# Optimization experiments

Hardware: AMD Instinct MI355X
Metric: run time of the kernel (lower is better)

Reference implementation:

```python
import jax, jax.numpy as jnp
import numpy as np

H = 256          # hidden_dim
ITERS = 3        # num_routing_iterations
# directed level pairs (src != tgt), torch iteration order over 3 levels:
SRC = jnp.array([0, 0, 1, 1, 2, 2])
TGT = jnp.array([1, 2, 0, 2, 0, 1])


def _ln(x, g, b, eps=1e-5):
    mu = x.mean(-1, keepdims=True)
    var = ((x - mu) ** 2).mean(-1, keepdims=True)
    return (x - mu) / jnp.sqrt(var + eps) * g + b


def setup_inputs() -> dict:
    key = jax.random.key(0)
    ks = iter(jax.random.split(key, 24))
    B = 32768
    lin = lambda k, fin, fout: jax.random.normal(k, (fin, fout), jnp.float32) / np.sqrt(fin).astype(np.float32)
    return {
        'x_fine':   jax.random.normal(next(ks), (B, 128), jnp.float32),
        'x_medium': jax.random.normal(next(ks), (B, 256), jnp.float32),
        'x_coarse': jax.random.normal(next(ks), (B, 512), jnp.float32),
        # per-level input projections (dims differ, so separate)
        'pW0': lin(next(ks), 128, H), 'pb0': jnp.zeros((H,), jnp.float32),
        'pW1': lin(next(ks), 256, H), 'pb1': jnp.zeros((H,), jnp.float32),
        'pW2': lin(next(ks), 512, H), 'pb2': jnp.zeros((H,), jnp.float32),
        # routing MLPs, stacked over the 6 directed pairs
        'rW1': jax.random.normal(next(ks), (6, 2 * H, H), jnp.float32) / np.sqrt(2 * H).astype(np.float32),
        'rb1': jnp.zeros((6, H), jnp.float32),
        'rW2': jax.random.normal(next(ks), (6, H, 1), jnp.float32) / np.sqrt(H).astype(np.float32),
        'rb2': jnp.zeros((6, 1), jnp.float32),
        # per-level processors, stacked over 3 levels
        'lpW1': jax.random.normal(next(ks), (3, H, H), jnp.float32) / np.sqrt(H).astype(np.float32),
        'lpb1': jnp.zeros((3, H), jnp.float32),
        'lpW2': jax.random.normal(next(ks), (3, H, H), jnp.float32) / np.sqrt(H).astype(np.float32),
        'lpb2': jnp.zeros((3, H), jnp.float32),
        'lng': jnp.ones((3, H), jnp.float32), 'lnb': jnp.zeros((3, H), jnp.float32),
        # final aggregator
        'faW1': jax.random.normal(next(ks), (3 * H, H), jnp.float32) / np.sqrt(3 * H).astype(np.float32),
        'fab1': jnp.zeros((H,), jnp.float32),
        'faW2': jax.random.normal(next(ks), (H, H), jnp.float32) / np.sqrt(H).astype(np.float32),
        'fab2': jnp.zeros((H,), jnp.float32),
        'fng': jnp.ones((H,), jnp.float32), 'fnb': jnp.zeros((H,), jnp.float32),
    }


def _forward(x_fine, x_medium, x_coarse, pW0, pb0, pW1, pb1, pW2, pb2,
             rW1, rb1, rW2, rb2, lpW1, lpb1, lpW2, lpb2, lng, lnb,
             faW1, fab1, faW2, fab2, fng, fnb):
    # project each level to hidden dim -> [3, B, H]
    feats = jnp.stack([x_fine @ pW0 + pb0,
                       x_medium @ pW1 + pb1,
                       x_coarse @ pW2 + pb2])
    w = None
    for _ in range(ITERS):  # fixed small routing-iteration loop
        src = feats[SRC]                                      # [6, B, H]
        tgt = feats[TGT]                                      # [6, B, H]
        comb = jnp.concatenate([src, tgt], axis=-1)           # [6, B, 2H]
        h = jax.nn.relu(jnp.einsum('pbd,pdh->pbh', comb, rW1) + rb1[:, None, :])
        w = jax.nn.sigmoid(jnp.einsum('pbh,pho->pbo', h, rW2) + rb2[:, None, :])  # [6, B, 1]
        # scatter routed features into target levels (weighted sum)
        agg = jax.ops.segment_sum(w * src, TGT, num_segments=3)  # [3, B, H]
        upd = feats + agg
        # per-level processor MLP + LayerNorm (dropout in eval mode = identity)
        h2 = jax.nn.relu(jnp.einsum('lbd,lde->lbe', upd, lpW1) + lpb1[:, None, :])
        h3 = jnp.einsum('lbd,lde->lbe', h2, lpW2) + lpb2[:, None, :]
        feats = _ln(h3, lng[:, None, :], lnb[:, None, :])
    B = feats.shape[1]
    cat = jnp.transpose(feats, (1, 0, 2)).reshape(B, 3 * H)  # level order matches torch cat
    h4 = jax.nn.relu(cat @ faW1 + fab1)
    out = _ln(h4 @ faW2 + fab2, fng, fnb)
    return out, w


def reference(x_fine, x_medium, x_coarse, pW0, pb0, pW1, pb1, pW2, pb2,
              rW1, rb1, rW2, rb2, lpW1, lpb1, lpW2, lpb2, lng, lnb,
              faW1, fab1, faW2, fab2, fng, fnb):
    return _forward(x_fine, x_medium, x_coarse, pW0, pb0, pW1, pb1, pW2, pb2,
                    rW1, rb1, rW2, rb2, lpW1, lpb1, lpW2, lpb2, lng, lnb,
                    faW1, fab1, faW2, fab2, fng, fnb)
```

## Files before the change

kernel.cpp:

```cpp
#include <hip/hip_runtime.h>
#include <math.h>

typedef __bf16 bf16;
typedef __bf16 bf16x8 __attribute__((ext_vector_type(8)));
typedef __bf16 bf16x4 __attribute__((ext_vector_type(4)));
typedef float f32x4 __attribute__((ext_vector_type(4)));

#define B_ROWS 32768
#define PSZ 8192
#define PBYTES 16384

#define PB_PW0   0
#define PB_PW1   4
#define PB_PW2   12
#define PB_RW1   28
#define PB_LPW1  124
#define PB_LPW2  148
#define PB_FAW1  172
#define PB_FAW2  196

__global__ void wprep_kernel(const float* __restrict__ pW0, const float* __restrict__ pW1,
                             const float* __restrict__ pW2, const float* __restrict__ rW1,
                             const float* __restrict__ lpW1, const float* __restrict__ lpW2,
                             const float* __restrict__ faW1, const float* __restrict__ faW2,
                             bf16* __restrict__ ws) {
  int p = blockIdx.x;
  const float* src; int kp;
  if (p < 4)        { src = pW0;  kp = p; }
  else if (p < 12)  { src = pW1;  kp = p - 4; }
  else if (p < 28)  { src = pW2;  kp = p - 12; }
  else if (p < 124) { int q = p - 28;  src = rW1  + (size_t)(q >> 4) * 512 * 256; kp = q & 15; }
  else if (p < 148) { int q = p - 124; src = lpW1 + (size_t)(q >> 3) * 256 * 256; kp = q & 7; }
  else if (p < 172) { int q = p - 148; src = lpW2 + (size_t)(q >> 3) * 256 * 256; kp = q & 7; }
  else if (p < 196) { src = faW1; kp = p - 172; }
  else              { src = faW2; kp = p - 196; }
  bf16* dst = ws + (size_t)p * PSZ;
  int n = threadIdx.x;
#pragma unroll
  for (int kb = 0; kb < 32; kb += 8) {
    bf16x8 v;
#pragma unroll
    for (int j = 0; j < 8; j++)
      v[j] = (bf16)src[(size_t)(kp * 32 + kb + j) * 256 + n];
    *(bf16x8*)(dst + n * 32 + kb) = v;
  }
}

#define FENCE asm volatile("" ::: "memory")
#define BAR()  do { FENCE; __builtin_amdgcn_s_barrier(); FENCE; } while (0)
#define BARP() do { asm volatile("s_waitcnt lgkmcnt(0)" ::: "memory"); \
                    __builtin_amdgcn_s_barrier(); FENCE; } while (0)
#define VWB2(N, B) asm volatile("s_waitcnt vmcnt(" #N ")" \
                                : "+v"(B[0]), "+v"(B[1]) :: "memory")
#define VWB4(N, B) asm volatile("s_waitcnt vmcnt(" #N ")" \
                                : "+v"(B[0]), "+v"(B[1]), "+v"(B[2]), "+v"(B[3]) :: "memory")

__device__ __forceinline__ void ld2(bf16x8& d0, bf16x8& d1, const void* addr) {
  asm volatile("global_load_dwordx4 %0, %2, off\n\t"
               "global_load_dwordx4 %1, %2, off offset:1024"
               : "=&v"(d0), "=&v"(d1)
               : "v"(addr));
}
__device__ __forceinline__ void ld4(bf16x8& d0, bf16x8& d1, bf16x8& d2, bf16x8& d3,
                                    const void* addr) {
  asm volatile("global_load_dwordx4 %0, %4, off\n\t"
               "global_load_dwordx4 %1, %4, off offset:1024\n\t"
               "global_load_dwordx4 %2, %4, off offset:2048\n\t"
               "global_load_dwordx4 %3, %4, off offset:3072"
               : "=&v"(d0), "=&v"(d1), "=&v"(d2), "=&v"(d3)
               : "v"(addr));
}

__global__ void __launch_bounds__(512)
__attribute__((amdgpu_waves_per_eu(2, 2)))
fused_kernel(const float* __restrict__ xf, const float* __restrict__ xm,
                  const float* __restrict__ xc,
                  const float* __restrict__ pb0, const float* __restrict__ pb1v,
                  const float* __restrict__ pb2v,
                  const float* __restrict__ rb1, const float* __restrict__ rW2,
                  const float* __restrict__ rb2,
                  const float* __restrict__ lpb1, const float* __restrict__ lpb2,
                  const float* __restrict__ lng, const float* __restrict__ lnb,
                  const float* __restrict__ fab1, const float* __restrict__ fab2,
                  const float* __restrict__ fng, const float* __restrict__ fnb,
                  const bf16* __restrict__ ws, float* __restrict__ out) {
  __shared__ bf16 feats[3][64][256];
  __shared__ bf16 apan[64][32];
  __shared__ float w_route[6][64];
  __shared__ float lnred[8][2][64];

  const int t = threadIdx.x;
  const int lane = t & 63;
  const int cg = t >> 6;
  const int lr = lane & 15;
  const int lk = lane >> 4;
  const int r0 = blockIdx.x * 64;

  char* featsB = (char*)&feats[0][0][0];
  char* apanB  = (char*)&apan[0][0];

  f32x4 acc[16];
  auto zacc16 = [&]() {
#pragma unroll
    for (int i = 0; i < 16; i++) acc[i] = (f32x4){0.f, 0.f, 0.f, 0.f};
  };
  auto zacc8 = [&]() {
#pragma unroll
    for (int i = 0; i < 8; i++) acc[i] = (f32x4){0.f, 0.f, 0.f, 0.f};
  };

  auto mf = [&](bf16x8* Av, bf16x8* Bv) {
    __builtin_amdgcn_s_setprio(1);
#pragma unroll
    for (int rt = 0; rt < 4; rt++)
#pragma unroll
      for (int ct = 0; ct < 2; ct++)
        acc[rt * 2 + ct] = __builtin_amdgcn_mfma_f32_16x16x32_bf16(Av[rt], Bv[ct], acc[rt * 2 + ct], 0, 0, 0);
    __builtin_amdgcn_s_setprio(0);
  };
  auto mfR = [&](bf16x8* Av, bf16x8* Bv) {
    __builtin_amdgcn_s_setprio(1);
#pragma unroll
    for (int rt = 0; rt < 4; rt++)
#pragma unroll
      for (int ct = 0; ct < 4; ct++)
        acc[rt * 4 + ct] = __builtin_amdgcn_mfma_f32_16x16x32_bf16(Av[rt], Bv[ct], acc[rt * 4 + ct], 0, 0, 0);
    __builtin_amdgcn_s_setprio(0);
  };

  const int SRCa[6] = {0, 0, 1, 1, 2, 2};
  const int TGTa[6] = {1, 2, 0, 2, 0, 1};

  auto gemmR = [&](int p0) {
    const int pp = p0 + (cg >> 2);
    const char* Wb = (const char*)(ws + (size_t)(PB_RW1 + pp * 16) * PSZ)
                     + (((cg & 3) * 64 + lr) * 64 + lk * 16);
    const int lS = SRCa[p0];
    const int lT = TGTa[pp];
    bf16x8 Ba[4], Bb[4], Aa[4], Ab[4];
    auto ldB = [&](int s, bf16x8* Bv) {
      ld4(Bv[0], Bv[1], Bv[2], Bv[3], Wb + (size_t)s * PBYTES);
    };
    auto readA = [&](int s, bf16x8* Av) {
      int lvl = (s < 8) ? lS : lT;
      int q = (s & 7) * 4;
#pragma unroll
      for (int rt = 0; rt < 4; rt++) {
        int r = rt * 16 + lr;
        Av[rt] = *(const bf16x8*)(featsB + ((lvl * 64 + r) << 9) + (((q + lk) ^ (r & 7)) << 4));
      }
    };
    ldB(0, Ba); ldB(1, Bb);
    readA(0, Aa);
    int s = 0;
#pragma unroll 1
    for (; s < 14; s += 2) {
      readA(s + 1, Ab); VWB4(4, Ba); mfR(Aa, Ba); ldB(s + 2, Ba);
      readA(s + 2, Aa); VWB4(4, Bb); mfR(Ab, Bb); ldB(s + 3, Bb);
    }
    readA(15, Ab); VWB4(4, Ba); mfR(Aa, Ba);
    VWB4(0, Bb); mfR(Ab, Bb);
  };

  auto routing_epi2 = [&](int p0) {
    const int pp = p0 + (cg >> 2);
    float part[4][4] = {{0}};
#pragma unroll
    for (int ct = 0; ct < 4; ct++) {
      int col = (cg & 3) * 64 + ct * 16 + lr;
      float b1 = rb1[pp * 256 + col];
      float w2 = rW2[pp * 256 + col];
#pragma unroll
      for (int rt = 0; rt < 4; rt++)
#pragma unroll
        for (int e = 0; e < 4; e++)
          part[rt][e] += fmaxf(acc[rt * 4 + ct][e] + b1, 0.f) * w2;
    }
#pragma unroll
    for (int m = 1; m < 16; m <<= 1)
#pragma unroll
      for (int rt = 0; rt < 4; rt++)
#pragma unroll
        for (int e = 0; e < 4; e++)
          part[rt][e] += __shfl_xor(part[rt][e], m, 64);
    if (lr == 0)
#pragma unroll
      for (int rt = 0; rt < 4; rt++)
#pragma unroll
        for (int e = 0; e < 4; e++)
          lnred[cg][0][rt * 16 + lk * 4 + e] = part[rt][e];
    BARP();
    if (t < 128) {
      int pi = t >> 6, r = t & 63;
      float s = rb2[p0 + pi];
#pragma unroll
      for (int g = 0; g < 4; g++) s += lnred[pi * 4 + g][0][r];
      w_route[p0 + pi][r] = 1.f / (1.f + expf(-s));
    }
    BARP();
  };

  auto gemm = [&](const bf16* W, int n, int l0, int l1, int l2) {
    const char* Wb = (const char*)W + ((cg * 32 + lr) * 64 + lk * 16);
    bf16x8 B0[2], B1[2], B2[2], B3[2], A0[4], A1[4];
    auto ldB = [&](int s, bf16x8* Bv) {
      ld2(Bv[0], Bv[1], Wb + (size_t)s * PBYTES);
    };
    auto readA = [&](int s, bf16x8* Av) {
      int lvl = (s >= 16) ? l2 : ((s >= 8) ? l1 : l0);
      int q = (s & 7) * 4;
#pragma unroll
      for (int rt = 0; rt < 4; rt++) {
        int r = rt * 16 + lr;
        Av[rt] = *(const bf16x8*)(featsB + ((lvl * 64 + r) << 9) + (((q + lk) ^ (r & 7)) << 4));
      }
    };
    ldB(0, B0); ldB(1, B1); ldB(2, B2); ldB(3, B3);
    readA(0, A0);
    int s = 0;
#pragma unroll 1
    for (; s < n - 4; s += 4) {
      readA(s + 1, A1); VWB2(6, B0); mf(A0, B0); ldB(s + 4, B0);
      readA(s + 2, A0); VWB2(6, B1); mf(A1, B1); ldB(s + 5, B1);
      readA(s + 3, A1); VWB2(6, B2); mf(A0, B2); ldB(s + 6, B2);
      readA(s + 4, A0); VWB2(6, B3); mf(A1, B3); ldB(s + 7, B3);
    }
    readA(s + 1, A1); VWB2(6, B0); mf(A0, B0);
    readA(s + 2, A0); VWB2(4, B1); mf(A1, B1);
    readA(s + 3, A1); VWB2(2, B2); mf(A0, B2);
    VWB2(0, B3); mf(A1, B3);
  };

  auto gemm_x = [&](const bf16* W, int n, const float* X, int Kx) {
    const char* Wb = (const char*)W + ((cg * 32 + lr) * 64 + lk * 16);
#pragma unroll 1
    for (int s = 0; s < n; s++) {
      bf16x8 b[2];
#pragma unroll
      for (int ct = 0; ct < 2; ct++)
        b[ct] = *(const bf16x8*)(Wb + (size_t)s * PBYTES + ct * 1024);
      int rr = t >> 3, c0 = (t & 7) * 4;
      float4 xv = *(const float4*)(X + (size_t)(r0 + rr) * Kx + s * 32 + c0);
      BAR();
      bf16x4 v;
      v[0] = (bf16)xv.x; v[1] = (bf16)xv.y; v[2] = (bf16)xv.z; v[3] = (bf16)xv.w;
      int cb = c0 >> 3;
      *(bf16x4*)(apanB + (rr << 6) + ((cb ^ ((rr >> 1) & 3)) << 4) + (c0 & 7) * 2) = v;
      BARP();
      bf16x8 a[4];
#pragma unroll
      for (int rt = 0; rt < 4; rt++) {
        int r = rt * 16 + lr;
        a[rt] = *(const bf16x8*)(apanB + (r << 6) + ((lk ^ ((r >> 1) & 3)) << 4));
      }
      mf(a, b);
    }
  };

  auto stF = [&](int lvl, int r, int c, float v) {
    *(bf16*)(featsB + ((lvl * 64 + r) << 9) +
             ((((c >> 3) ^ (r & 7))) << 4) + (c & 7) * 2) = (bf16)v;
  };
  auto epi_bias_store = [&](const float* bias, int lvl, bool do_relu) {
    BAR();
#pragma unroll
    for (int ct = 0; ct < 2; ct++) {
      int col = cg * 32 + ct * 16 + lr;
      float bv = bias[col];
#pragma unroll
      for (int rt = 0; rt < 4; rt++)
#pragma unroll
        for (int e = 0; e < 4; e++) {
          float v = acc[rt * 2 + ct][e] + bv;
          if (do_relu) v = fmaxf(v, 0.f);
          stF(lvl, rt * 16 + lk * 4 + e, col, v);
        }
    }
    BARP();
  };
  auto ln_epi = [&](const float* bias, const float* gamma, const float* beta, int lvl) {
    float sum[4][4] = {{0}}, sq[4][4] = {{0}};
#pragma unroll
    for (int ct = 0; ct < 2; ct++) {
      int col = cg * 32 + ct * 16 + lr;
      float bv = bias[col];
#pragma unroll
      for (int rt = 0; rt < 4; rt++)
#pragma unroll
        for (int e = 0; e < 4; e++) {
          float v = acc[rt * 2 + ct][e] + bv;
          acc[rt * 2 + ct][e] = v;
          sum[rt][e] += v; sq[rt][e] += v * v;
        }
    }
#pragma unroll
    for (int m = 1; m < 16; m <<= 1)
#pragma unroll
      for (int rt = 0; rt < 4; rt++)
#pragma unroll
        for (int e = 0; e < 4; e++) {
          sum[rt][e] += __shfl_xor(sum[rt][e], m, 64);
          sq[rt][e]  += __shfl_xor(sq[rt][e], m, 64);
        }
    if (lr == 0)
#pragma unroll
      for (int rt = 0; rt < 4; rt++)
#pragma unroll
        for (int e = 0; e < 4; e++) {
          int r = rt * 16 + lk * 4 + e;
          lnred[cg][0][r] = sum[rt][e];
          lnred[cg][1][r] = sq[rt][e];
        }
    BARP();
    if (t < 64) {
      float su = 0.f, sz = 0.f;
#pragma unroll
      for (int g = 0; g < 8; g++) { su += lnred[g][0][t]; sz += lnred[g][1][t]; }
      float mu = su * (1.f / 256.f);
      float ms = sz * (1.f / 256.f);
      lnred[0][0][t] = mu;
      lnred[0][1][t] = rsqrtf(ms - mu * mu + 1e-5f);
    }
    BARP();
#pragma unroll
    for (int rt = 0; rt < 4; rt++)
#pragma unroll
      for (int e = 0; e < 4; e++) {
        int r = rt * 16 + lk * 4 + e;
        float mu = lnred[0][0][r];
        float rstd = lnred[0][1][r];
#pragma unroll
        for (int ct = 0; ct < 2; ct++) {
          int col = cg * 32 + ct * 16 + lr;
          float v = (acc[rt * 2 + ct][e] - mu) * rstd * gamma[col] + beta[col];
          if (lvl >= 0) stF(lvl, r, col, v);
          else out[(size_t)(r0 + r) * 256 + col] = v;
        }
      }
    BARP();
  };

  zacc8(); gemm_x(ws + PB_PW0 * PSZ, 4,  xf, 128); epi_bias_store(pb0, 0, false);
  zacc8(); gemm_x(ws + PB_PW1 * PSZ, 8,  xm, 256); epi_bias_store(pb1v, 1, false);
  zacc8(); gemm_x(ws + PB_PW2 * PSZ, 16, xc, 512); epi_bias_store(pb2v, 2, false);

  for (int it = 0; it < 3; it++) {
    for (int p0 = 0; p0 < 6; p0 += 2) {
      zacc16();
      gemmR(p0);
      routing_epi2(p0);
    }
    {
      int r = t >> 3, c0 = (t & 7) * 32;
      float w6[6];
#pragma unroll
      for (int p = 0; p < 6; p++) w6[p] = w_route[p][r];
#pragma unroll
      for (int ccx = 0; ccx < 32; ccx += 8) {
        int c = c0 + ccx;
        int chunk = (((c >> 3) ^ (r & 7)) << 4);
        char* a0 = featsB + ((0 * 64 + r) << 9) + chunk;
        char* a1 = featsB + ((1 * 64 + r) << 9) + chunk;
        char* a2 = featsB + ((2 * 64 + r) << 9) + chunk;
        bf16x8 f0 = *(bf16x8*)a0, f1 = *(bf16x8*)a1, f2 = *(bf16x8*)a2;
        bf16x8 u0, u1, u2;
#pragma unroll
        for (int i = 0; i < 8; i++) {
          float a = (float)f0[i], b = (float)f1[i], d = (float)f2[i];
          u0[i] = (bf16)(a + w6[2] * b + w6[4] * d);
          u1[i] = (bf16)(b + w6[0] * a + w6[5] * d);
          u2[i] = (bf16)(d + w6[1] * a + w6[3] * b);
        }
        *(bf16x8*)a0 = u0; *(bf16x8*)a1 = u1; *(bf16x8*)a2 = u2;
      }
      BARP();
    }
    for (int l = 0; l < 3; l++) {
      zacc8();
      gemm(ws + (PB_LPW1 + l * 8) * PSZ, 8, l, 0, 0);
      epi_bias_store(lpb1 + l * 256, l, true);
      zacc8();
      gemm(ws + (PB_LPW2 + l * 8) * PSZ, 8, l, 0, 0);
      ln_epi(lpb2 + l * 256, lng + l * 256, lnb + l * 256, l);
    }
  }

  zacc8();
  gemm(ws + PB_FAW1 * PSZ, 24, 0, 1, 2);
  epi_bias_store(fab1, 0, true);
  zacc8();
  gemm(ws + PB_FAW2 * PSZ, 8, 0, 0, 0);
  ln_epi(fab2, fng, fnb, -1);

  if (t < 384) {
    int p = t >> 6, r = t & 63;
    out[(size_t)B_ROWS * 256 + (size_t)p * B_ROWS + r0 + r] = w_route[p][r];
  }
}

extern "C" void kernel_launch(void* const* d_in, const int* in_sizes, int n_in,
                              void* d_out, int out_size, void* d_ws, size_t ws_size,
                              hipStream_t stream) {
  const float* xf   = (const float*)d_in[0];
  const float* xm   = (const float*)d_in[1];
  const float* xc   = (const float*)d_in[2];
  const float* pW0  = (const float*)d_in[3];
  const float* pb0  = (const float*)d_in[4];
  const float* pW1  = (const float*)d_in[5];
  const float* pb1  = (const float*)d_in[6];
  const float* pW2  = (const float*)d_in[7];
  const float* pb2  = (const float*)d_in[8];
  const float* rW1  = (const float*)d_in[9];
  const float* rb1  = (const float*)d_in[10];
  const float* rW2  = (const float*)d_in[11];
  const float* rb2  = (const float*)d_in[12];
  const float* lpW1 = (const float*)d_in[13];
  const float* lpb1 = (const float*)d_in[14];
  const float* lpW2 = (const float*)d_in[15];
  const float* lpb2 = (const float*)d_in[16];
  const float* lng  = (const float*)d_in[17];
  const float* lnb  = (const float*)d_in[18];
  const float* faW1 = (const float*)d_in[19];
  const float* fab1 = (const float*)d_in[20];
  const float* faW2 = (const float*)d_in[21];
  const float* fab2 = (const float*)d_in[22];
  const float* fng  = (const float*)d_in[23];
  const float* fnb  = (const float*)d_in[24];
  (void)in_sizes; (void)n_in; (void)out_size; (void)ws_size;

  bf16* ws = (bf16*)d_ws;
  float* out = (float*)d_out;

  wprep_kernel<<<204, 256, 0, stream>>>(pW0, pW1, pW2, rW1, lpW1, lpW2, faW1, faW2, ws);
  fused_kernel<<<512, 512, 0, stream>>>(xf, xm, xc, pb0, pb1, pb2, rb1, rW2, rb2,
                                        lpb1, lpb2, lng, lnb, fab1, fab2, fng, fnb,
                                        ws, out);
}
```

Baseline: 425.9 us.

## Halve row tile to 32 rows per block to double occupancy

```diff
diff --git a/kernel.cpp b/kernel.cpp
--- a/kernel.cpp
+++ b/kernel.cpp
@@ -4,6 +4,7 @@
 typedef __bf16 bf16;
 typedef __bf16 bf16x8 __attribute__((ext_vector_type(8)));
 typedef __bf16 bf16x4 __attribute__((ext_vector_type(4)));
+typedef __bf16 bf16x2 __attribute__((ext_vector_type(2)));
 typedef float f32x4 __attribute__((ext_vector_type(4)));
 
 #define B_ROWS 32768
@@ -72,7 +73,7 @@
 }
 
 __global__ void __launch_bounds__(512)
-__attribute__((amdgpu_waves_per_eu(2, 2)))
+__attribute__((amdgpu_waves_per_eu(4, 4)))
 fused_kernel(const float* __restrict__ xf, const float* __restrict__ xm,
                   const float* __restrict__ xc,
                   const float* __restrict__ pb0, const float* __restrict__ pb1v,
@@ -84,35 +85,35 @@
                   const float* __restrict__ fab1, const float* __restrict__ fab2,
                   const float* __restrict__ fng, const float* __restrict__ fnb,
                   const bf16* __restrict__ ws, float* __restrict__ out) {
-  __shared__ bf16 feats[3][64][256];
-  __shared__ bf16 apan[64][32];
-  __shared__ float w_route[6][64];
-  __shared__ float lnred[8][2][64];
+  __shared__ bf16 feats[3][32][256];
+  __shared__ char scratch[2048];
+  __shared__ float w_route[6][32];
 
   const int t = threadIdx.x;
   const int lane = t & 63;
   const int cg = t >> 6;
   const int lr = lane & 15;
   const int lk = lane >> 4;
-  const int r0 = blockIdx.x * 64;
+  const int r0 = blockIdx.x * 32;
 
   char* featsB = (char*)&feats[0][0][0];
-  char* apanB  = (char*)&apan[0][0];
-
-  f32x4 acc[16];
-  auto zacc16 = [&]() {
-#pragma unroll
-    for (int i = 0; i < 16; i++) acc[i] = (f32x4){0.f, 0.f, 0.f, 0.f};
-  };
+  char* apanB  = scratch;
+  float (*lnred)[2][32] = (float (*)[2][32])scratch;
+
+  f32x4 acc[8];
   auto zacc8 = [&]() {
 #pragma unroll
     for (int i = 0; i < 8; i++) acc[i] = (f32x4){0.f, 0.f, 0.f, 0.f};
+  };
+  auto zacc4 = [&]() {
+#pragma unroll
+    for (int i = 0; i < 4; i++) acc[i] = (f32x4){0.f, 0.f, 0.f, 0.f};
   };
 
   auto mf = [&](bf16x8* Av, bf16x8* Bv) {
     __builtin_amdgcn_s_setprio(1);
 #pragma unroll
-    for (int rt = 0; rt < 4; rt++)
+    for (int rt = 0; rt < 2; rt++)
 #pragma unroll
       for (int ct = 0; ct < 2; ct++)
         acc[rt * 2 + ct] = __builtin_amdgcn_mfma_f32_16x16x32_bf16(Av[rt], Bv[ct], acc[rt * 2 + ct], 0, 0, 0);
@@ -121,7 +122,7 @@
   auto mfR = [&](bf16x8* Av, bf16x8* Bv) {
     __builtin_amdgcn_s_setprio(1);
 #pragma unroll
-    for (int rt = 0; rt < 4; rt++)
+    for (int rt = 0; rt < 2; rt++)
 #pragma unroll
       for (int ct = 0; ct < 4; ct++)
         acc[rt * 4 + ct] = __builtin_amdgcn_mfma_f32_16x16x32_bf16(Av[rt], Bv[ct], acc[rt * 4 + ct], 0, 0, 0);
@@ -137,7 +138,7 @@
                      + (((cg & 3) * 64 + lr) * 64 + lk * 16);
     const int lS = SRCa[p0];
     const int lT = TGTa[pp];
-    bf16x8 Ba[4], Bb[4], Aa[4], Ab[4];
+    bf16x8 Ba[4], Bb[4], Aa[2], Ab[2];
     auto ldB = [&](int s, bf16x8* Bv) {
       ld4(Bv[0], Bv[1], Bv[2], Bv[3], Wb + (size_t)s * PBYTES);
     };
@@ -145,9 +146,9 @@
       int lvl = (s < 8) ? lS : lT;
       int q = (s & 7) * 4;
 #pragma unroll
-      for (int rt = 0; rt < 4; rt++) {
+      for (int rt = 0; rt < 2; rt++) {
         int r = rt * 16 + lr;
-        Av[rt] = *(const bf16x8*)(featsB + ((lvl * 64 + r) << 9) + (((q + lk) ^ (r & 7)) << 4));
+        Av[rt] = *(const bf16x8*)(featsB + ((lvl * 32 + r) << 9) + (((q + lk) ^ (r & 7)) << 4));
       }
     };
     ldB(0, Ba); ldB(1, Bb);
@@ -164,14 +165,14 @@
 
   auto routing_epi2 = [&](int p0) {
     const int pp = p0 + (cg >> 2);
-    float part[4][4] = {{0}};
+    float part[2][4] = {{0}};
 #pragma unroll
     for (int ct = 0; ct < 4; ct++) {
       int col = (cg & 3) * 64 + ct * 16 + lr;
       float b1 = rb1[pp * 256 + col];
       float w2 = rW2[pp * 256 + col];
 #pragma unroll
-      for (int rt = 0; rt < 4; rt++)
+      for (int rt = 0; rt < 2; rt++)
 #pragma unroll
         for (int e = 0; e < 4; e++)
           part[rt][e] += fmaxf(acc[rt * 4 + ct][e] + b1, 0.f) * w2;
@@ -179,19 +180,19 @@
 #pragma unroll
     for (int m = 1; m < 16; m <<= 1)
 #pragma unroll
-      for (int rt = 0; rt < 4; rt++)
+      for (int rt = 0; rt < 2; rt++)
 #pragma unroll
         for (int e = 0; e < 4; e++)
           part[rt][e] += __shfl_xor(part[rt][e], m, 64);
     if (lr == 0)
 #pragma unroll
-      for (int rt = 0; rt < 4; rt++)
+      for (int rt = 0; rt < 2; rt++)
 #pragma unroll
         for (int e = 0; e < 4; e++)
           lnred[cg][0][rt * 16 + lk * 4 + e] = part[rt][e];
     BARP();
-    if (t < 128) {
-      int pi = t >> 6, r = t & 63;
+    if (t < 64) {
+      int pi = t >> 5, r = t & 31;
       float s = rb2[p0 + pi];
 #pragma unroll
       for (int g = 0; g < 4; g++) s += lnred[pi * 4 + g][0][r];
@@ -202,7 +203,7 @@
 
   auto gemm = [&](const bf16* W, int n, int l0, int l1, int l2) {
     const char* Wb = (const char*)W + ((cg * 32 + lr) * 64 + lk * 16);
-    bf16x8 B0[2], B1[2], B2[2], B3[2], A0[4], A1[4];
+    bf16x8 B0[2], B1[2], B2[2], B3[2], A0[2], A1[2];
     auto ldB = [&](int s, bf16x8* Bv) {
       ld2(Bv[0], Bv[1], Wb + (size_t)s * PBYTES);
     };
@@ -210,9 +211,9 @@
       int lvl = (s >= 16) ? l2 : ((s >= 8) ? l1 : l0);
       int q = (s & 7) * 4;
 #pragma unroll
-      for (int rt = 0; rt < 4; rt++) {
+      for (int rt = 0; rt < 2; rt++) {
         int r = rt * 16 + lr;
-        Av[rt] = *(const bf16x8*)(featsB + ((lvl * 64 + r) << 9) + (((q + lk) ^ (r & 7)) << 4));
+        Av[rt] = *(const bf16x8*)(featsB + ((lvl * 32 + r) << 9) + (((q + lk) ^ (r & 7)) << 4));
       }
     };
     ldB(0, B0); ldB(1, B1); ldB(2, B2); ldB(3, B3);
@@ -239,17 +240,17 @@
 #pragma unroll
       for (int ct = 0; ct < 2; ct++)
         b[ct] = *(const bf16x8*)(Wb + (size_t)s * PBYTES + ct * 1024);
-      int rr = t >> 3, c0 = (t & 7) * 4;
-      float4 xv = *(const float4*)(X + (size_t)(r0 + rr) * Kx + s * 32 + c0);
+      int rr = t >> 4, c0 = (t & 15) * 2;
+      float2 xv = *(const float2*)(X + (size_t)(r0 + rr) * Kx + s * 32 + c0);
       BAR();
-      bf16x4 v;
-      v[0] = (bf16)xv.x; v[1] = (bf16)xv.y; v[2] = (bf16)xv.z; v[3] = (bf16)xv.w;
+      bf16x2 v;
+      v[0] = (bf16)xv.x; v[1] = (bf16)xv.y;
       int cb = c0 >> 3;
-      *(bf16x4*)(apanB + (rr << 6) + ((cb ^ ((rr >> 1) & 3)) << 4) + (c0 & 7) * 2) = v;
+      *(bf16x2*)(apanB + (rr << 6) + ((cb ^ ((rr >> 1) & 3)) << 4) + (c0 & 7) * 2) = v;
       BARP();
-      bf16x8 a[4];
-#pragma unroll
-      for (int rt = 0; rt < 4; rt++) {
+      bf16x8 a[2];
+#pragma unroll
+      for (int rt = 0; rt < 2; rt++) {
         int r = rt * 16 + lr;
         a[rt] = *(const bf16x8*)(apanB + (r << 6) + ((lk ^ ((r >> 1) & 3)) << 4));
       }
@@ -258,7 +259,7 @@
   };
 
   auto stF = [&](int lvl, int r, int c, float v) {
-    *(bf16*)(featsB + ((lvl * 64 + r) << 9) +
+    *(bf16*)(featsB + ((lvl * 32 + r) << 9) +
              ((((c >> 3) ^ (r & 7))) << 4) + (c & 7) * 2) = (bf16)v;
   };
   auto epi_bias_store = [&](const float* bias, int lvl, bool do_relu) {
@@ -268,7 +269,7 @@
       int col = cg * 32 + ct * 16 + lr;
       float bv = bias[col];
 #pragma unroll
-      for (int rt = 0; rt < 4; rt++)
+      for (int rt = 0; rt < 2; rt++)
 #pragma unroll
         for (int e = 0; e < 4; e++) {
           float v = acc[rt * 2 + ct][e] + bv;
@@ -279,13 +280,13 @@
     BARP();
   };
   auto ln_epi = [&](const float* bias, const float* gamma, const float* beta, int lvl) {
-    float sum[4][4] = {{0}}, sq[4][4] = {{0}};
+    float sum[2][4] = {{0}}, sq[2][4] = {{0}};
 #pragma unroll
     for (int ct = 0; ct < 2; ct++) {
       int col = cg * 32 + ct * 16 + lr;
       float bv = bias[col];
 #pragma unroll
-      for (int rt = 0; rt < 4; rt++)
+      for (int rt = 0; rt < 2; rt++)
 #pragma unroll
         for (int e = 0; e < 4; e++) {
           float v = acc[rt * 2 + ct][e] + bv;
@@ -296,15 +297,15 @@
 #pragma unroll
     for (int m = 1; m < 16; m <<= 1)
 #pragma unroll
-      for (int rt = 0; rt < 4; rt++)
-#pragma unroll
-        for (int e = 0; e < 4; e++) {
+      for (int rt = 0; rt < 2; rt++)
+#pragma unroll
+      for (int e = 0; e < 4; e++) {
           sum[rt][e] += __shfl_xor(sum[rt][e], m, 64);
           sq[rt][e]  += __shfl_xor(sq[rt][e], m, 64);
         }
     if (lr == 0)
 #pragma unroll
-      for (int rt = 0; rt < 4; rt++)
+      for (int rt = 0; rt < 2; rt++)
 #pragma unroll
         for (int e = 0; e < 4; e++) {
           int r = rt * 16 + lk * 4 + e;
@@ -312,7 +313,7 @@
           lnred[cg][1][r] = sq[rt][e];
         }
     BARP();
-    if (t < 64) {
+    if (t < 32) {
       float su = 0.f, sz = 0.f;
 #pragma unroll
       for (int g = 0; g < 8; g++) { su += lnred[g][0][t]; sz += lnred[g][1][t]; }
@@ -323,7 +324,7 @@
     }
     BARP();
 #pragma unroll
-    for (int rt = 0; rt < 4; rt++)
+    for (int rt = 0; rt < 2; rt++)
 #pragma unroll
       for (int e = 0; e < 4; e++) {
         int r = rt * 16 + lk * 4 + e;
@@ -340,28 +341,28 @@
     BARP();
   };
 
-  zacc8(); gemm_x(ws + PB_PW0 * PSZ, 4,  xf, 128); epi_bias_store(pb0, 0, false);
-  zacc8(); gemm_x(ws + PB_PW1 * PSZ, 8,  xm, 256); epi_bias_store(pb1v, 1, false);
-  zacc8(); gemm_x(ws + PB_PW2 * PSZ, 16, xc, 512); epi_bias_store(pb2v, 2, false);
+  zacc4(); gemm_x(ws + PB_PW0 * PSZ, 4,  xf, 128); epi_bias_store(pb0, 0, false);
+  zacc4(); gemm_x(ws + PB_PW1 * PSZ, 8,  xm, 256); epi_bias_store(pb1v, 1, false);
+  zacc4(); gemm_x(ws + PB_PW2 * PSZ, 16, xc, 512); epi_bias_store(pb2v, 2, false);
 
   for (int it = 0; it < 3; it++) {
     for (int p0 = 0; p0 < 6; p0 += 2) {
-      zacc16();
+      zacc8();
       gemmR(p0);
       routing_epi2(p0);
     }
     {
-      int r = t >> 3, c0 = (t & 7) * 32;
+      int r = t >> 4, c0 = (t & 15) * 16;
       float w6[6];
 #pragma unroll
       for (int p = 0; p < 6; p++) w6[p] = w_route[p][r];
 #pragma unroll
-      for (int ccx = 0; ccx < 32; ccx += 8) {
+      for (int ccx = 0; ccx < 16; ccx += 8) {
         int c = c0 + ccx;
         int chunk = (((c >> 3) ^ (r & 7)) << 4);
-        char* a0 = featsB + ((0 * 64 + r) << 9) + chunk;
-        char* a1 = featsB + ((1 * 64 + r) << 9) + chunk;
-        char* a2 = featsB + ((2 * 64 + r) << 9) + chunk;
+        char* a0 = featsB + ((0 * 32 + r) << 9) + chunk;
+        char* a1 = featsB + ((1 * 32 + r) << 9) + chunk;
+        char* a2 = featsB + ((2 * 32 + r) << 9) + chunk;
         bf16x8 f0 = *(bf16x8*)a0, f1 = *(bf16x8*)a1, f2 = *(bf16x8*)a2;
         bf16x8 u0, u1, u2;
 #pragma unroll
@@ -376,24 +377,24 @@
       BARP();
     }
     for (int l = 0; l < 3; l++) {
-      zacc8();
+      zacc4();
       gemm(ws + (PB_LPW1 + l * 8) * PSZ, 8, l, 0, 0);
       epi_bias_store(lpb1 + l * 256, l, true);
-      zacc8();
+      zacc4();
       gemm(ws + (PB_LPW2 + l * 8) * PSZ, 8, l, 0, 0);
       ln_epi(lpb2 + l * 256, lng + l * 256, lnb + l * 256, l);
     }
   }
 
-  zacc8();
+  zacc4();
   gemm(ws + PB_FAW1 * PSZ, 24, 0, 1, 2);
   epi_bias_store(fab1, 0, true);
-  zacc8();
+  zacc4();
   gemm(ws + PB_FAW2 * PSZ, 8, 0, 0, 0);
   ln_epi(fab2, fng, fnb, -1);
 
-  if (t < 384) {
-    int p = t >> 6, r = t & 63;
+  if (t < 192) {
+    int p = t >> 5, r = t & 31;
     out[(size_t)B_ROWS * 256 + (size_t)p * B_ROWS + r0 + r] = w_route[p][r];
   }
 }
@@ -432,7 +433,7 @@
   float* out = (float*)d_out;
 
   wprep_kernel<<<204, 256, 0, stream>>>(pW0, pW1, pW2, rW1, lpW1, lpW2, faW1, faW2, ws);
-  fused_kernel<<<512, 512, 0, stream>>>(xf, xm, xc, pb0, pb1, pb2, rb1, rW2, rb2,
-                                        lpb1, lpb2, lng, lnb, fab1, fab2, fng, fnb,
-                                        ws, out);
+  fused_kernel<<<1024, 512, 0, stream>>>(xf, xm, xc, pb0, pb1, pb2, rb1, rW2, rb2,
+                                         lpb1, lpb2, lng, lnb, fab1, fab2, fng, fnb,
+                                         ws, out);
 }
```

Result: slower. 636.2 us (+49.4%).

## Shrink per-block row tile to 48 and relax waves-per-EU bound

Applied to the files above, without the earlier changes.

```diff
diff --git a/kernel.cpp b/kernel.cpp
--- a/kernel.cpp
+++ b/kernel.cpp
@@ -7,6 +7,7 @@
 typedef float f32x4 __attribute__((ext_vector_type(4)));
 
 #define B_ROWS 32768
+#define ROWS 48
 #define PSZ 8192
 #define PBYTES 16384
 
@@ -72,7 +73,7 @@
 }
 
 __global__ void __launch_bounds__(512)
-__attribute__((amdgpu_waves_per_eu(2, 2)))
+__attribute__((amdgpu_waves_per_eu(2, 4)))
 fused_kernel(const float* __restrict__ xf, const float* __restrict__ xm,
                   const float* __restrict__ xc,
                   const float* __restrict__ pb0, const float* __restrict__ pb1v,
@@ -84,35 +85,35 @@
                   const float* __restrict__ fab1, const float* __restrict__ fab2,
                   const float* __restrict__ fng, const float* __restrict__ fnb,
                   const bf16* __restrict__ ws, float* __restrict__ out) {
-  __shared__ bf16 feats[3][64][256];
-  __shared__ bf16 apan[64][32];
-  __shared__ float w_route[6][64];
-  __shared__ float lnred[8][2][64];
+  __shared__ bf16 feats[3][ROWS][256];
+  __shared__ char scratch[3072];
+  __shared__ float w_route[6][ROWS];
 
   const int t = threadIdx.x;
   const int lane = t & 63;
   const int cg = t >> 6;
   const int lr = lane & 15;
   const int lk = lane >> 4;
-  const int r0 = blockIdx.x * 64;
+  const int r0 = blockIdx.x * ROWS;
 
   char* featsB = (char*)&feats[0][0][0];
-  char* apanB  = (char*)&apan[0][0];
-
-  f32x4 acc[16];
-  auto zacc16 = [&]() {
-#pragma unroll
-    for (int i = 0; i < 16; i++) acc[i] = (f32x4){0.f, 0.f, 0.f, 0.f};
-  };
-  auto zacc8 = [&]() {
-#pragma unroll
-    for (int i = 0; i < 8; i++) acc[i] = (f32x4){0.f, 0.f, 0.f, 0.f};
+  char* apanB  = scratch;
+  float (*lnred)[2][ROWS] = (float (*)[2][ROWS])scratch;
+
+  f32x4 acc[12];
+  auto zacc12 = [&]() {
+#pragma unroll
+    for (int i = 0; i < 12; i++) acc[i] = (f32x4){0.f, 0.f, 0.f, 0.f};
+  };
+  auto zacc6 = [&]() {
+#pragma unroll
+    for (int i = 0; i < 6; i++) acc[i] = (f32x4){0.f, 0.f, 0.f, 0.f};
   };
 
   auto mf = [&](bf16x8* Av, bf16x8* Bv) {
     __builtin_amdgcn_s_setprio(1);
 #pragma unroll
-    for (int rt = 0; rt < 4; rt++)
+    for (int rt = 0; rt < 3; rt++)
 #pragma unroll
       for (int ct = 0; ct < 2; ct++)
         acc[rt * 2 + ct] = __builtin_amdgcn_mfma_f32_16x16x32_bf16(Av[rt], Bv[ct], acc[rt * 2 + ct], 0, 0, 0);
@@ -121,7 +122,7 @@
   auto mfR = [&](bf16x8* Av, bf16x8* Bv) {
     __builtin_amdgcn_s_setprio(1);
 #pragma unroll
-    for (int rt = 0; rt < 4; rt++)
+    for (int rt = 0; rt < 3; rt++)
 #pragma unroll
       for (int ct = 0; ct < 4; ct++)
         acc[rt * 4 + ct] = __builtin_amdgcn_mfma_f32_16x16x32_bf16(Av[rt], Bv[ct], acc[rt * 4 + ct], 0, 0, 0);
@@ -137,7 +138,7 @@
                      + (((cg & 3) * 64 + lr) * 64 + lk * 16);
     const int lS = SRCa[p0];
     const int lT = TGTa[pp];
-    bf16x8 Ba[4], Bb[4], Aa[4], Ab[4];
+    bf16x8 Ba[4], Bb[4], Aa[3], Ab[3];
     auto ldB = [&](int s, bf16x8* Bv) {
       ld4(Bv[0], Bv[1], Bv[2], Bv[3], Wb + (size_t)s * PBYTES);
     };
@@ -145,9 +146,9 @@
       int lvl = (s < 8) ? lS : lT;
       int q = (s & 7) * 4;
 #pragma unroll
-      for (int rt = 0; rt < 4; rt++) {
+      for (int rt = 0; rt < 3; rt++) {
         int r = rt * 16 + lr;
-        Av[rt] = *(const bf16x8*)(featsB + ((lvl * 64 + r) << 9) + (((q + lk) ^ (r & 7)) << 4));
+        Av[rt] = *(const bf16x8*)(featsB + ((lvl * ROWS + r) << 9) + (((q + lk) ^ (r & 7)) << 4));
       }
     };
     ldB(0, Ba); ldB(1, Bb);
@@ -164,14 +165,14 @@
 
   auto routing_epi2 = [&](int p0) {
     const int pp = p0 + (cg >> 2);
-    float part[4][4] = {{0}};
+    float part[3][4] = {{0}};
 #pragma unroll
     for (int ct = 0; ct < 4; ct++) {
       int col = (cg & 3) * 64 + ct * 16 + lr;
       float b1 = rb1[pp * 256 + col];
       float w2 = rW2[pp * 256 + col];
 #pragma unroll
-      for (int rt = 0; rt < 4; rt++)
+      for (int rt = 0; rt < 3; rt++)
 #pragma unroll
         for (int e = 0; e < 4; e++)
           part[rt][e] += fmaxf(acc[rt * 4 + ct][e] + b1, 0.f) * w2;
@@ -179,19 +180,19 @@
 #pragma unroll
     for (int m = 1; m < 16; m <<= 1)
 #pragma unroll
-      for (int rt = 0; rt < 4; rt++)
+      for (int rt = 0; rt < 3; rt++)
 #pragma unroll
         for (int e = 0; e < 4; e++)
           part[rt][e] += __shfl_xor(part[rt][e], m, 64);
     if (lr == 0)
 #pragma unroll
-      for (int rt = 0; rt < 4; rt++)
+      for (int rt = 0; rt < 3; rt++)
 #pragma unroll
         for (int e = 0; e < 4; e++)
           lnred[cg][0][rt * 16 + lk * 4 + e] = part[rt][e];
     BARP();
-    if (t < 128) {
-      int pi = t >> 6, r = t & 63;
+    if (t < 2 * ROWS) {
+      int pi = t / ROWS, r = t % ROWS;
       float s = rb2[p0 + pi];
 #pragma unroll
       for (int g = 0; g < 4; g++) s += lnred[pi * 4 + g][0][r];
@@ -202,7 +203,7 @@
 
   auto gemm = [&](const bf16* W, int n, int l0, int l1, int l2) {
     const char* Wb = (const char*)W + ((cg * 32 + lr) * 64 + lk * 16);
-    bf16x8 B0[2], B1[2], B2[2], B3[2], A0[4], A1[4];
+    bf16x8 B0[2], B1[2], B2[2], B3[2], A0[3], A1[3];
     auto ldB = [&](int s, bf16x8* Bv) {
       ld2(Bv[0], Bv[1], Wb + (size_t)s * PBYTES);
     };
@@ -210,9 +211,9 @@
       int lvl = (s >= 16) ? l2 : ((s >= 8) ? l1 : l0);
       int q = (s & 7) * 4;
 #pragma unroll
-      for (int rt = 0; rt < 4; rt++) {
+      for (int rt = 0; rt < 3; rt++) {
         int r = rt * 16 + lr;
-        Av[rt] = *(const bf16x8*)(featsB + ((lvl * 64 + r) << 9) + (((q + lk) ^ (r & 7)) << 4));
+        Av[rt] = *(const bf16x8*)(featsB + ((lvl * ROWS + r) << 9) + (((q + lk) ^ (r & 7)) << 4));
       }
     };
     ldB(0, B0); ldB(1, B1); ldB(2, B2); ldB(3, B3);
@@ -233,23 +234,26 @@
 
   auto gemm_x = [&](const bf16* W, int n, const float* X, int Kx) {
     const char* Wb = (const char*)W + ((cg * 32 + lr) * 64 + lk * 16);
+    int rr = t >> 3, c0 = (t & 7) * 4;
+    int row = r0 + rr; if (row > B_ROWS - 1) row = B_ROWS - 1;
 #pragma unroll 1
     for (int s = 0; s < n; s++) {
       bf16x8 b[2];
 #pragma unroll
       for (int ct = 0; ct < 2; ct++)
         b[ct] = *(const bf16x8*)(Wb + (size_t)s * PBYTES + ct * 1024);
-      int rr = t >> 3, c0 = (t & 7) * 4;
-      float4 xv = *(const float4*)(X + (size_t)(r0 + rr) * Kx + s * 32 + c0);
+      float4 xv = *(const float4*)(X + (size_t)row * Kx + s * 32 + c0);
       BAR();
-      bf16x4 v;
-      v[0] = (bf16)xv.x; v[1] = (bf16)xv.y; v[2] = (bf16)xv.z; v[3] = (bf16)xv.w;
-      int cb = c0 >> 3;
-      *(bf16x4*)(apanB + (rr << 6) + ((cb ^ ((rr >> 1) & 3)) << 4) + (c0 & 7) * 2) = v;
+      if (rr < ROWS) {
+        bf16x4 v;
+        v[0] = (bf16)xv.x; v[1] = (bf16)xv.y; v[2] = (bf16)xv.z; v[3] = (bf16)xv.w;
+        int cb = c0 >> 3;
+        *(bf16x4*)(apanB + (rr << 6) + ((cb ^ ((rr >> 1) & 3)) << 4) + (c0 & 7) * 2) = v;
+      }
       BARP();
-      bf16x8 a[4];
-#pragma unroll
-      for (int rt = 0; rt < 4; rt++) {
+      bf16x8 a[3];
+#pragma unroll
+      for (int rt = 0; rt < 3; rt++) {
         int r = rt * 16 + lr;
         a[rt] = *(const bf16x8*)(apanB + (r << 6) + ((lk ^ ((r >> 1) & 3)) << 4));
       }
@@ -258,7 +262,7 @@
   };
 
   auto stF = [&](int lvl, int r, int c, float v) {
-    *(bf16*)(featsB + ((lvl * 64 + r) << 9) +
+    *(bf16*)(featsB + ((lvl * ROWS + r) << 9) +
              ((((c >> 3) ^ (r & 7))) << 4) + (c & 7) * 2) = (bf16)v;
   };
   auto epi_bias_store = [&](const float* bias, int lvl, bool do_relu) {
@@ -268,7 +272,7 @@
       int col = cg * 32 + ct * 16 + lr;
       float bv = bias[col];
 #pragma unroll
-      for (int rt = 0; rt < 4; rt++)
+      for (int rt = 0; rt < 3; rt++)
 #pragma unroll
         for (int e = 0; e < 4; e++) {
           float v = acc[rt * 2 + ct][e] + bv;
@@ -279,13 +283,13 @@
     BARP();
   };
   auto ln_epi = [&](const float* bias, const float* gamma, const float* beta, int lvl) {
-    float sum[4][4] = {{0}}, sq[4][4] = {{0}};
+    float sum[3][4] = {{0}}, sq[3][4] = {{0}};
 #pragma unroll
     for (int ct = 0; ct < 2; ct++) {
       int col = cg * 32 + ct * 16 + lr;
       float bv = bias[col];
 #pragma unroll
-      for (int rt = 0; rt < 4; rt++)
+      for (int rt = 0; rt < 3; rt++)
 #pragma unroll
         for (int e = 0; e < 4; e++) {
           float v = acc[rt * 2 + ct][e] + bv;
@@ -296,7 +300,7 @@
 #pragma unroll
     for (int m = 1; m < 16; m <<= 1)
 #pragma unroll
-      for (int rt = 0; rt < 4; rt++)
+      for (int rt = 0; rt < 3; rt++)
 #pragma unroll
         for (int e = 0; e < 4; e++) {
           sum[rt][e] += __shfl_xor(sum[rt][e], m, 64);
@@ -304,7 +308,7 @@
         }
     if (lr == 0)
 #pragma unroll
-      for (int rt = 0; rt < 4; rt++)
+      for (int rt = 0; rt < 3; rt++)
 #pragma unroll
         for (int e = 0; e < 4; e++) {
           int r = rt * 16 + lk * 4 + e;
@@ -312,7 +316,7 @@
           lnred[cg][1][r] = sq[rt][e];
         }
     BARP();
-    if (t < 64) {
+    if (t < ROWS) {
       float su = 0.f, sz = 0.f;
 #pragma unroll
       for (int g = 0; g < 8; g++) { su += lnred[g][0][t]; sz += lnred[g][1][t]; }
@@ -323,7 +327,7 @@
     }
     BARP();
 #pragma unroll
-    for (int rt = 0; rt < 4; rt++)
+    for (int rt = 0; rt < 3; rt++)
 #pragma unroll
       for (int e = 0; e < 4; e++) {
         int r = rt * 16 + lk * 4 + e;
@@ -334,67 +338,70 @@
           int col = cg * 32 + ct * 16 + lr;
           float v = (acc[rt * 2 + ct][e] - mu) * rstd * gamma[col] + beta[col];
           if (lvl >= 0) stF(lvl, r, col, v);
-          else out[(size_t)(r0 + r) * 256 + col] = v;
-        }
-      }
-    BARP();
-  };
-
-  zacc8(); gemm_x(ws + PB_PW0 * PSZ, 4,  xf, 128); epi_bias_store(pb0, 0, false);
-  zacc8(); gemm_x(ws + PB_PW1 * PSZ, 8,  xm, 256); epi_bias_store(pb1v, 1, false);
-  zacc8(); gemm_x(ws + PB_PW2 * PSZ, 16, xc, 512); epi_bias_store(pb2v, 2, false);
+          else if (r0 + r < B_ROWS) out[(size_t)(r0 + r) * 256 + col] = v;
+        }
+      }
+    BARP();
+  };
+
+  zacc6(); gemm_x(ws + PB_PW0 * PSZ, 4,  xf, 128); epi_bias_store(pb0, 0, false);
+  zacc6(); gemm_x(ws + PB_PW1 * PSZ, 8,  xm, 256); epi_bias_store(pb1v, 1, false);
+  zacc6(); gemm_x(ws + PB_PW2 * PSZ, 16, xc, 512); epi_bias_store(pb2v, 2, false);
 
   for (int it = 0; it < 3; it++) {
     for (int p0 = 0; p0 < 6; p0 += 2) {
-      zacc16();
+      zacc12();
       gemmR(p0);
       routing_epi2(p0);
     }
     {
       int r = t >> 3, c0 = (t & 7) * 32;
-      float w6[6];
-#pragma unroll
-      for (int p = 0; p < 6; p++) w6[p] = w_route[p][r];
-#pragma unroll
-      for (int ccx = 0; ccx < 32; ccx += 8) {
-        int c = c0 + ccx;
-        int chunk = (((c >> 3) ^ (r & 7)) << 4);
-        char* a0 = featsB + ((0 * 64 + r) << 9) + chunk;
-        char* a1 = featsB + ((1 * 64 + r) << 9) + chunk;
-        char* a2 = featsB + ((2 * 64 + r) << 9) + chunk;
-        bf16x8 f0 = *(bf16x8*)a0, f1 = *(bf16x8*)a1, f2 = *(bf16x8*)a2;
-        bf16x8 u0, u1, u2;
-#pragma unroll
-        for (int i = 0; i < 8; i++) {
-          float a = (float)f0[i], b = (float)f1[i], d = (float)f2[i];
-          u0[i] = (bf16)(a + w6[2] * b + w6[4] * d);
-          u1[i] = (bf16)(b + w6[0] * a + w6[5] * d);
-          u2[i] = (bf16)(d + w6[1] * a + w6[3] * b);
-        }
-        *(bf16x8*)a0 = u0; *(bf16x8*)a1 = u1; *(bf16x8*)a2 = u2;
+      if (r < ROWS) {
+        float w6[6];
+#pragma unroll
+        for (int p = 0; p < 6; p++) w6[p] = w_route[p][r];
+#pragma unroll
+        for (int ccx = 0; ccx < 32; ccx += 8) {
+          int c = c0 + ccx;
+          int chunk = (((c >> 3) ^ (r & 7)) << 4);
+          char* a0 = featsB + ((0 * ROWS + r) << 9) + chunk;
+          char* a1 = featsB + ((1 * ROWS + r) << 9) + chunk;
+          char* a2 = featsB + ((2 * ROWS + r) << 9) + chunk;
+          bf16x8 f0 = *(bf16x8*)a0, f1 = *(bf16x8*)a1, f2 = *(bf16x8*)a2;
+          bf16x8 u0, u1, u2;
+#pragma unroll
+          for (int i = 0; i < 8; i++) {
+            float a = (float)f0[i], b = (float)f1[i], d = (float)f2[i];
+            u0[i] = (bf16)(a + w6[2] * b + w6[4] * d);
+            u1[i] = (bf16)(b + w6[0] * a + w6[5] * d);
+            u2[i] = (bf16)(d + w6[1] * a + w6[3] * b);
+          }
+          *(bf16x8*)a0 = u0; *(bf16x8*)a1 = u1; *(bf16x8*)a2 = u2;
+        }
       }
       BARP();
     }
     for (int l = 0; l < 3; l++) {
-      zacc8();
+      zacc6();
       gemm(ws + (PB_LPW1 + l * 8) * PSZ, 8, l, 0, 0);
       epi_bias_store(lpb1 + l * 256, l, true);
-      zacc8();
+      zacc6();
       gemm(ws + (PB_LPW2 + l * 8) * PSZ, 8, l, 0, 0);
       ln_epi(lpb2 + l * 256, lng + l * 256, lnb + l * 256, l);
     }
   }
 
-  zacc8();
+  zacc6();
   gemm(ws + PB_FAW1 * PSZ, 24, 0, 1, 2);
   epi_bias_store(fab1, 0, true);
-  zacc8();
+  zacc6();
   gemm(ws + PB_FAW2 * PSZ, 8, 0, 0, 0);
   ln_epi(fab2, fng, fnb, -1);
 
-  if (t < 384) {
-    int p = t >> 6, r = t & 63;
-    out[(size_t)B_ROWS * 256 + (size_t)p * B_ROWS + r0 + r] = w_route[p][r];
+  if (t < 6 * ROWS) {
+    int p = t / ROWS, r = t % ROWS;
+    if (r0 + r < B_ROWS)
+      out[(size_t)B_ROWS * 256 + (size_t)p * B_ROWS + r0 + r] = w_route[p][r];
   }
 }
 
@@ -431,8 +438,9 @@
   bf16* ws = (bf16*)d_ws;
   float* out = (float*)d_out;
 
+  int nblk = (B_ROWS + ROWS - 1) / ROWS;
   wprep_kernel<<<204, 256, 0, stream>>>(pW0, pW1, pW2, rW1, lpW1, lpW2, faW1, faW2, ws);
-  fused_kernel<<<512, 512, 0, stream>>>(xf, xm, xc, pb0, pb1, pb2, rb1, rW2, rb2,
-                                        lpb1, lpb2, lng, lnb, fab1, fab2, fng, fnb,
-                                        ws, out);
+  fused_kernel<<<nblk, 512, 0, stream>>>(xf, xm, xc, pb0, pb1, pb2, rb1, rW2, rb2,
+                                         lpb1, lpb2, lng, lnb, fab1, fab2, fng, fnb,
+                                         ws, out);
 }
```

Measured after the change: 563.9 us. 32.4% more time.
